# Optimization experiments

Hardware: AMD Instinct MI355X
Metric: run time of the kernel (lower is better)

Reference implementation:

```python
import jax, jax.numpy as jnp
import numpy as np

N, A, B, K = 100000, 64, 128, 27  # active sites, in/out channels, 3^3 offsets
EPS = 1e-4  # scn BatchNorm default eps
LEAK = 0.0  # leakiness=0 -> ReLU


def bn_lrelu(x, gamma, beta):
    # training-mode BN over active sites, fused leaky relu
    mu = x.mean(0)
    var = x.var(0)
    xh = (x - mu) * jax.lax.rsqrt(var + EPS) * gamma + beta
    return jnp.where(xh > 0, xh, LEAK * xh)


def subconv(f, nbr, mask, W):
    # submanifold conv via rulebook: f [N,Cin], nbr [N,K], mask [N,K], W [K,Cin,Cout]
    out = jnp.zeros((f.shape[0], W.shape[2]), f.dtype)
    for k in range(W.shape[0]):  # fixed small set of kernel offsets
        g = jnp.where(mask[:, k:k + 1], f[nbr[:, k]], jnp.zeros((), f.dtype))
        out = out + g @ W[k]
    return out


def setup_inputs() -> dict:
    key = jax.random.key(0)
    ks = jax.random.split(key, 8)
    feat = jax.random.normal(ks[0], (N, A), jnp.float32)
    nbr = jax.random.randint(ks[1], (N, K), 0, N, jnp.int32)
    mask = jax.random.randint(ks[2], (N, K), 0, 2, jnp.int32).astype(bool)
    # self-connection at center offset is always valid in submanifold conv
    center = K // 2
    nbr = nbr.at[:, center].set(jnp.arange(N, dtype=jnp.int32))
    mask = mask.at[:, center].set(True)
    s1 = 1.0 / np.sqrt(K * A)
    s2 = 1.0 / np.sqrt(K * B)
    W1 = jax.random.normal(ks[3], (K, A, B), jnp.float32) * s1
    W2 = jax.random.normal(ks[4], (K, B, B), jnp.float32) * s2
    Wnin = jax.random.normal(ks[5], (A, B), jnp.float32) / np.sqrt(A)
    gamma1 = jnp.ones((A,), jnp.float32)
    beta1 = jnp.zeros((A,), jnp.float32)
    gamma2 = jnp.ones((B,), jnp.float32)
    beta2 = jnp.zeros((B,), jnp.float32)
    return {"feat": feat, "gamma1": gamma1, "beta1": beta1, "W1": W1,
            "gamma2": gamma2, "beta2": beta2, "W2": W2, "Wnin": Wnin,
            "nbr": nbr, "mask": mask}


def reference(feat, gamma1, beta1, W1, gamma2, beta2, W2, Wnin, nbr, mask):
    y1 = feat @ Wnin  # NetworkInNetwork shortcut (a != b)
    h = bn_lrelu(feat, gamma1, beta1)
    h = subconv(h, nbr, mask, W1)
    h = bn_lrelu(h, gamma2, beta2)
    y2 = subconv(h, nbr, mask, W2)
    return y1 + y2  # add_feature_planes
```

## Files before the change

### kernel.cpp

```cpp
#include <hip/hip_runtime.h>
#include <stdint.h>

#define CA 64
#define CB 128
#define KOFF 27
#define BN_EPS 1e-4f

typedef short bf16x8 __attribute__((ext_vector_type(8)));
typedef float f32x4 __attribute__((ext_vector_type(4)));
typedef unsigned int u32x4 __attribute__((ext_vector_type(4)));
typedef unsigned short u16x4 __attribute__((ext_vector_type(4)));

__device__ __forceinline__ unsigned short f2bf(float f) {
  union { float f; uint32_t u; } c; c.f = f;
  uint32_t u = c.u;
  return (unsigned short)((u + 0x7FFFu + ((u >> 16) & 1u)) >> 16);
}

__global__ void detect_mask_k(const unsigned char* __restrict__ m, int* flag) {
  unsigned v = 0;
  for (int i = threadIdx.x; i < 4096; i += 256)
    if (i & 3) v |= m[i];
  if (v) atomicOr(flag, 1);
}

__global__ void pack_mask_k(const void* __restrict__ mp, const int* __restrict__ flag,
                            uint32_t* __restrict__ bits, int n) {
  int i = blockIdx.x * blockDim.x + threadIdx.x;
  if (i >= n) return;
  uint32_t b = 0;
  if (*flag) {
    const unsigned char* m = (const unsigned char*)mp + (size_t)i * KOFF;
    for (int k = 0; k < KOFF; k++) b |= (m[k] ? 1u : 0u) << k;
  } else {
    const int* m = (const int*)mp + (size_t)i * KOFF;
    for (int k = 0; k < KOFF; k++) b |= (m[k] ? 1u : 0u) << k;
  }
  bits[i] = b;
}

__global__ void transpose_w_k(const float* __restrict__ w, unsigned short* __restrict__ wt,
                              int K, int Cin, int Cout) {
  int idx = blockIdx.x * blockDim.x + threadIdx.x;
  int total = K * Cin * Cout;
  if (idx >= total) return;
  int ci = idx % Cin;
  int t2 = idx / Cin;
  int co = t2 % Cout;
  int k  = t2 / Cout;
  wt[idx] = f2bf(w[((size_t)k * Cin + ci) * Cout + co]);
}

template<int C>
__global__ void col_stats_k(const float* __restrict__ x, int n, float* __restrict__ sums) {
  __shared__ float ssum[C], ssq[C];
  int t = threadIdx.x;
  for (int i = t; i < C; i += 256) { ssum[i] = 0.f; ssq[i] = 0.f; }
  __syncthreads();
  const int c = t % C;
  const int rpb = 256 / C;
  float s = 0.f, q = 0.f;
  for (int r = blockIdx.x * rpb + t / C; r < n; r += gridDim.x * rpb) {
    float v = x[(size_t)r * C + c];
    s += v; q += v * v;
  }
  atomicAdd(&ssum[c], s);
  atomicAdd(&ssq[c], q);
  __syncthreads();
  for (int i = t; i < C; i += 256) {
    atomicAdd(&sums[i], ssum[i]);
    atomicAdd(&sums[C + i], ssq[i]);
  }
}

template<int C>
__global__ void bn_finalize_k(const float* __restrict__ sums, const float* __restrict__ gamma,
                              const float* __restrict__ beta, float* __restrict__ sc, int n) {
  int c = threadIdx.x;
  if (c >= C) return;
  float inv_n = 1.f / (float)n;
  float mean = sums[c] * inv_n;
  float var = sums[C + c] * inv_n - mean * mean;
  float rstd = rsqrtf(var + BN_EPS);
  float scale = gamma[c] * rstd;
  sc[c] = scale;
  sc[C + c] = beta[c] - mean * scale;
}

template<int C, bool RAW>
__global__ void bn_apply_k(const float* __restrict__ x, const float* __restrict__ sc,
                           unsigned short* __restrict__ h, unsigned short* __restrict__ raw,
                           int total) {
  int idx = (blockIdx.x * blockDim.x + threadIdx.x) * 4;
  if (idx >= total) return;
  f32x4 v = *(const f32x4*)&x[idx];
  int c0 = idx % C;
  u16x4 ho, ro;
#pragma unroll
  for (int j = 0; j < 4; j++) {
    float s = sc[c0 + j], b = sc[C + c0 + j];
    float hv = fmaxf(v[j] * s + b, 0.f);
    ho[j] = f2bf(hv);
    if (RAW) ro[j] = f2bf(v[j]);
  }
  *(u16x4*)&h[idx] = ho;
  if (RAW) *(u16x4*)&raw[idx] = ro;
}

template<int CIN, bool FUSE>
__launch_bounds__(256)
__global__ void conv_k(const unsigned short* __restrict__ hin,
                       const unsigned short* __restrict__ wt,
                       const int* __restrict__ nbr,
                       const uint32_t* __restrict__ mbits,
                       const unsigned short* __restrict__ fbraw,
                       const unsigned short* __restrict__ wnt,
                       float* __restrict__ out, int n) {
  constexpr int TR = 64;
  constexpr int STR = CIN + 8;
  constexpr int FSTR = CA + 8;
  __shared__ alignas(16) unsigned short tile[TR * STR];
  __shared__ alignas(16) unsigned short ftile[FUSE ? TR * FSTR : 16];
  __shared__ int lnbr[TR * KOFF];
  __shared__ uint32_t lmb[TR];

  const int t = threadIdx.x;
  const int rowbase = blockIdx.x * TR;
  const int nrows = min(TR, n - rowbase);

  for (int i = t; i < nrows * KOFF; i += 256) lnbr[i] = nbr[(size_t)rowbase * KOFF + i];
  if (t < TR) lmb[t] = (t < nrows) ? mbits[rowbase + t] : 0u;

  if constexpr (FUSE) {
#pragma unroll
    for (int p = 0; p < 2; p++) {
      int r = p * 32 + (t >> 3);
      int ch = (t & 7) * 8;
      u32x4 v = {0, 0, 0, 0};
      if (r < nrows) v = *(const u32x4*)&fbraw[(size_t)(rowbase + r) * CA + ch];
      *(u32x4*)&ftile[r * FSTR + ch] = v;
    }
  }
  __syncthreads();

  const int lane = t & 63;
  const int wave = t >> 6;
  const int l16 = lane & 15;
  const int quad = lane >> 4;
  const int colbase = wave * 32;

  f32x4 zero = {0.f, 0.f, 0.f, 0.f};
  f32x4 acc[4][2];
#pragma unroll
  for (int i = 0; i < 4; i++) { acc[i][0] = zero; acc[i][1] = zero; }

  if constexpr (FUSE) {
#pragma unroll
    for (int ks = 0; ks < CA / 32; ks++) {
      bf16x8 b0 = *(const bf16x8*)&wnt[(size_t)(colbase + l16) * CA + ks * 32 + quad * 8];
      bf16x8 b1 = *(const bf16x8*)&wnt[(size_t)(colbase + 16 + l16) * CA + ks * 32 + quad * 8];
#pragma unroll
      for (int rt = 0; rt < 4; rt++) {
        bf16x8 a = *(const bf16x8*)&ftile[(rt * 16 + l16) * FSTR + ks * 32 + quad * 8];
        acc[rt][0] = __builtin_amdgcn_mfma_f32_16x16x32_bf16(a, b0, acc[rt][0], 0, 0, 0);
        acc[rt][1] = __builtin_amdgcn_mfma_f32_16x16x32_bf16(a, b1, acc[rt][1], 0, 0, 0);
      }
    }
  }

  constexpr int CH = CIN / 8;
  constexpr int RPP = 256 / CH;

  for (int k = 0; k < KOFF; k++) {
#pragma unroll
    for (int p = 0; p < TR / RPP; p++) {
      int r = p * RPP + t / CH;
      int ch = (t % CH) * 8;
      u32x4 v = {0, 0, 0, 0};
      if (r < nrows && ((lmb[r] >> k) & 1u)) {
        int nb = lnbr[r * KOFF + k];
        v = *(const u32x4*)&hin[(size_t)nb * CIN + ch];
      }
      *(u32x4*)&tile[r * STR + ch] = v;
    }
    __syncthreads();
    const unsigned short* wk = wt + (size_t)k * CB * CIN;
#pragma unroll
    for (int ks = 0; ks < CIN / 32; ks++) {
      bf16x8 b0 = *(const bf16x8*)&wk[(size_t)(colbase + l16) * CIN + ks * 32 + quad * 8];
      bf16x8 b1 = *(const bf16x8*)&wk[(size_t)(colbase + 16 + l16) * CIN + ks * 32 + quad * 8];
#pragma unroll
      for (int rt = 0; rt < 4; rt++) {
        bf16x8 a = *(const bf16x8*)&tile[(rt * 16 + l16) * STR + ks * 32 + quad * 8];
        acc[rt][0] = __builtin_amdgcn_mfma_f32_16x16x32_bf16(a, b0, acc[rt][0], 0, 0, 0);
        acc[rt][1] = __builtin_amdgcn_mfma_f32_16x16x32_bf16(a, b1, acc[rt][1], 0, 0, 0);
      }
    }
    __syncthreads();
  }

#pragma unroll
  for (int rt = 0; rt < 4; rt++) {
#pragma unroll
    for (int ct = 0; ct < 2; ct++) {
#pragma unroll
      for (int i = 0; i < 4; i++) {
        int r = rt * 16 + quad * 4 + i;
        if (r < nrows) {
          int c = colbase + ct * 16 + l16;
          out[(size_t)(rowbase + r) * CB + c] = acc[rt][ct][i];
        }
      }
    }
  }
}

extern "C" void kernel_launch(void* const* d_in, const int* in_sizes, int n_in,
                              void* d_out, int out_size, void* d_ws, size_t ws_size,
                              hipStream_t stream) {
  const float* feat   = (const float*)d_in[0];
  const float* gamma1 = (const float*)d_in[1];
  const float* beta1  = (const float*)d_in[2];
  const float* W1     = (const float*)d_in[3];
  const float* gamma2 = (const float*)d_in[4];
  const float* beta2  = (const float*)d_in[5];
  const float* W2     = (const float*)d_in[6];
  const float* Wnin   = (const float*)d_in[7];
  const int*   nbr    = (const int*)d_in[8];
  const void*  mask   = d_in[9];
  float* out = (float*)d_out;

  const int n = in_sizes[0] / CA;

  char* ws = (char*)d_ws;
  size_t off = 0;
  auto alloc = [&](size_t bytes) { size_t p = off; off += (bytes + 255) & ~(size_t)255; return p; };
  int*            flag  = (int*)           (ws + alloc(256));
  float*          sums1 = (float*)         (ws + alloc(2 * CA * 4));
  float*          sums2 = (float*)         (ws + alloc(2 * CB * 4));
  float*          sc1   = (float*)         (ws + alloc(2 * CA * 4));
  float*          sc2   = (float*)         (ws + alloc(2 * CB * 4));
  uint32_t*       mbits = (uint32_t*)      (ws + alloc((size_t)n * 4));
  unsigned short* fb    = (unsigned short*)(ws + alloc((size_t)n * CA * 2));
  unsigned short* hb1   = (unsigned short*)(ws + alloc((size_t)n * CA * 2));
  float*          out1  = (float*)         (ws + alloc((size_t)n * CB * 4));
  unsigned short* hb2   = (unsigned short*)(ws + alloc((size_t)n * CB * 2));
  unsigned short* w1t   = (unsigned short*)(ws + alloc((size_t)KOFF * CB * CA * 2));
  unsigned short* w2t   = (unsigned short*)(ws + alloc((size_t)KOFF * CB * CB * 2));
  unsigned short* wnt   = (unsigned short*)(ws + alloc((size_t)CB * CA * 2));

  hipMemsetAsync(d_ws, 0, 1792, stream);

  detect_mask_k<<<1, 256, 0, stream>>>((const unsigned char*)mask, flag);
  pack_mask_k<<<(n + 255) / 256, 256, 0, stream>>>(mask, flag, mbits, n);

  {
    int t1 = KOFF * CA * CB, t2 = KOFF * CB * CB, t3 = CA * CB;
    transpose_w_k<<<(t1 + 255) / 256, 256, 0, stream>>>(W1, w1t, KOFF, CA, CB);
    transpose_w_k<<<(t2 + 255) / 256, 256, 0, stream>>>(W2, w2t, KOFF, CB, CB);
    transpose_w_k<<<(t3 + 255) / 256, 256, 0, stream>>>(Wnin, wnt, 1, CA, CB);
  }

  col_stats_k<CA><<<256, 256, 0, stream>>>(feat, n, sums1);
  bn_finalize_k<CA><<<1, CA, 0, stream>>>(sums1, gamma1, beta1, sc1, n);
  bn_apply_k<CA, true><<<(n * CA / 4 + 255) / 256, 256, 0, stream>>>(feat, sc1, hb1, fb, n * CA);

  conv_k<CA, false><<<(n + 63) / 64, 256, 0, stream>>>(hb1, w1t, nbr, mbits, nullptr, nullptr, out1, n);

  col_stats_k<CB><<<256, 256, 0, stream>>>(out1, n, sums2);
  bn_finalize_k<CB><<<1, CB, 0, stream>>>(sums2, gamma2, beta2, sc2, n);
  bn_apply_k<CB, false><<<(n * CB / 4 + 255) / 256, 256, 0, stream>>>(out1, sc2, hb2, nullptr, n * CB);

  conv_k<CB, true><<<(n + 63) / 64, 256, 0, stream>>>(hb2, w2t, nbr, mbits, fb, wnt, out, n);
}
```

Before: 606.5 us.

## Double-buffer gather tiles and prefetch weights in registers in sparse conv

The conv kernel now double-buffers the LDS gather tile. The neighbour rows for offset k+2 and the weight fragments for the next offsets are loaded into registers while the MFMAs for offset k run, so one barrier per offset replaces two. The barrier is a custom s_waitcnt lgkmcnt(0) plus s_barrier. This aims to hide the global gather and weight-load latency behind compute, at the cost of more registers and LDS that may lower occupancy. The three weight transpose launches are also merged into one kernel to cut launch overhead.

Result: faster. 531.1 us (-12.4%).

```diff
diff --git a/kernel.cpp b/kernel.cpp
--- a/kernel.cpp
+++ b/kernel.cpp
@@ -15,6 +15,10 @@
   union { float f; uint32_t u; } c; c.f = f;
   uint32_t u = c.u;
   return (unsigned short)((u + 0x7FFFu + ((u >> 16) & 1u)) >> 16);
+}
+
+__device__ __forceinline__ void barrier_lds() {
+  asm volatile("s_waitcnt lgkmcnt(0)\n\ts_barrier" ::: "memory");
 }
 
 __global__ void detect_mask_k(const unsigned char* __restrict__ m, int* flag) {
@@ -39,16 +43,24 @@
   bits[i] = b;
 }
 
-__global__ void transpose_w_k(const float* __restrict__ w, unsigned short* __restrict__ wt,
-                              int K, int Cin, int Cout) {
+__global__ void transpose_all_k(const float* __restrict__ W1, const float* __restrict__ W2,
+                                const float* __restrict__ Wnin,
+                                unsigned short* __restrict__ w1t, unsigned short* __restrict__ w2t,
+                                unsigned short* __restrict__ wnt) {
+  const int t1 = KOFF * CA * CB, t2 = KOFF * CB * CB, t3 = CA * CB;
   int idx = blockIdx.x * blockDim.x + threadIdx.x;
-  int total = K * Cin * Cout;
-  if (idx >= total) return;
-  int ci = idx % Cin;
-  int t2 = idx / Cin;
-  int co = t2 % Cout;
-  int k  = t2 / Cout;
-  wt[idx] = f2bf(w[((size_t)k * Cin + ci) * Cout + co]);
+  if (idx < t1) {
+    int ci = idx % CA; int r = idx / CA; int co = r % CB; int k = r / CB;
+    w1t[idx] = f2bf(W1[((size_t)k * CA + ci) * CB + co]);
+  } else if (idx < t1 + t2) {
+    int j = idx - t1;
+    int ci = j % CB; int r = j / CB; int co = r % CB; int k = r / CB;
+    w2t[j] = f2bf(W2[((size_t)k * CB + ci) * CB + co]);
+  } else if (idx < t1 + t2 + t3) {
+    int j = idx - t1 - t2;
+    int ci = j % CA; int co = j / CA;
+    wnt[j] = f2bf(Wnin[(size_t)ci * CB + co]);
+  }
 }
 
 template<int C>
@@ -119,7 +131,11 @@
   constexpr int TR = 64;
   constexpr int STR = CIN + 8;
   constexpr int FSTR = CA + 8;
-  __shared__ alignas(16) unsigned short tile[TR * STR];
+  constexpr int NKS = CIN / 32;
+  constexpr int CH = CIN / 8;
+  constexpr int NP = TR * CH / 256;
+
+  __shared__ alignas(16) unsigned short tile[2][TR * STR];
   __shared__ alignas(16) unsigned short ftile[FUSE ? TR * FSTR : 16];
   __shared__ int lnbr[TR * KOFF];
   __shared__ uint32_t lmb[TR];
@@ -148,17 +164,57 @@
   const int l16 = lane & 15;
   const int quad = lane >> 4;
   const int colbase = wave * 32;
-
-  f32x4 zero = {0.f, 0.f, 0.f, 0.f};
+  const int goff = (t % CH) * 8;
+  const int grow = t / CH;
+  const int boff0 = (colbase + l16) * CIN + quad * 8;
+  const int boff1 = boff0 + 16 * CIN;
+
   f32x4 acc[4][2];
 #pragma unroll
-  for (int i = 0; i < 4; i++) { acc[i][0] = zero; acc[i][1] = zero; }
+  for (int i = 0; i < 4; i++) { acc[i][0] = f32x4{0,0,0,0}; acc[i][1] = f32x4{0,0,0,0}; }
+
+  bf16x8 bfr[2][2 * NKS];
+  u32x4 gr[NP];
+
+#pragma unroll
+  for (int ks = 0; ks < NKS; ks++) {
+    bfr[0][2 * ks]     = *(const bf16x8*)&wt[boff0 + ks * 32];
+    bfr[0][2 * ks + 1] = *(const bf16x8*)&wt[boff1 + ks * 32];
+  }
+#pragma unroll
+  for (int p = 0; p < NP; p++) {
+    int r = p * (256 / CH) + grow;
+    u32x4 v = {0, 0, 0, 0};
+    if (r < nrows && (lmb[r] & 1u)) v = *(const u32x4*)&hin[(size_t)lnbr[r * KOFF] * CIN + goff];
+    gr[p] = v;
+  }
+#pragma unroll
+  for (int p = 0; p < NP; p++) {
+    int r = p * (256 / CH) + grow;
+    *(u32x4*)&tile[0][r * STR + goff] = gr[p];
+  }
+  {
+    const unsigned short* wk = wt + (size_t)1 * CB * CIN;
+#pragma unroll
+    for (int ks = 0; ks < NKS; ks++) {
+      bfr[1][2 * ks]     = *(const bf16x8*)&wk[boff0 + ks * 32];
+      bfr[1][2 * ks + 1] = *(const bf16x8*)&wk[boff1 + ks * 32];
+    }
+  }
+#pragma unroll
+  for (int p = 0; p < NP; p++) {
+    int r = p * (256 / CH) + grow;
+    u32x4 v = {0, 0, 0, 0};
+    if (r < nrows && ((lmb[r] >> 1) & 1u))
+      v = *(const u32x4*)&hin[(size_t)lnbr[r * KOFF + 1] * CIN + goff];
+    gr[p] = v;
+  }
 
   if constexpr (FUSE) {
 #pragma unroll
     for (int ks = 0; ks < CA / 32; ks++) {
-      bf16x8 b0 = *(const bf16x8*)&wnt[(size_t)(colbase + l16) * CA + ks * 32 + quad * 8];
-      bf16x8 b1 = *(const bf16x8*)&wnt[(size_t)(colbase + 16 + l16) * CA + ks * 32 + quad * 8];
+      bf16x8 b0 = *(const bf16x8*)&wnt[(colbase + l16) * CA + ks * 32 + quad * 8];
+      bf16x8 b1 = *(const bf16x8*)&wnt[(colbase + 16 + l16) * CA + ks * 32 + quad * 8];
 #pragma unroll
       for (int rt = 0; rt < 4; rt++) {
         bf16x8 a = *(const bf16x8*)&ftile[(rt * 16 + l16) * FSTR + ks * 32 + quad * 8];
@@ -167,36 +223,46 @@
       }
     }
   }
-
-  constexpr int CH = CIN / 8;
-  constexpr int RPP = 256 / CH;
-
+  barrier_lds();
+
+#pragma unroll
   for (int k = 0; k < KOFF; k++) {
-#pragma unroll
-    for (int p = 0; p < TR / RPP; p++) {
-      int r = p * RPP + t / CH;
-      int ch = (t % CH) * 8;
-      u32x4 v = {0, 0, 0, 0};
-      if (r < nrows && ((lmb[r] >> k) & 1u)) {
-        int nb = lnbr[r * KOFF + k];
-        v = *(const u32x4*)&hin[(size_t)nb * CIN + ch];
-      }
-      *(u32x4*)&tile[r * STR + ch] = v;
-    }
-    __syncthreads();
-    const unsigned short* wk = wt + (size_t)k * CB * CIN;
-#pragma unroll
-    for (int ks = 0; ks < CIN / 32; ks++) {
-      bf16x8 b0 = *(const bf16x8*)&wk[(size_t)(colbase + l16) * CIN + ks * 32 + quad * 8];
-      bf16x8 b1 = *(const bf16x8*)&wk[(size_t)(colbase + 16 + l16) * CIN + ks * 32 + quad * 8];
+    const int cur = k & 1, nxt = cur ^ 1;
+#pragma unroll
+    for (int ks = 0; ks < NKS; ks++) {
 #pragma unroll
       for (int rt = 0; rt < 4; rt++) {
-        bf16x8 a = *(const bf16x8*)&tile[(rt * 16 + l16) * STR + ks * 32 + quad * 8];
-        acc[rt][0] = __builtin_amdgcn_mfma_f32_16x16x32_bf16(a, b0, acc[rt][0], 0, 0, 0);
-        acc[rt][1] = __builtin_amdgcn_mfma_f32_16x16x32_bf16(a, b1, acc[rt][1], 0, 0, 0);
-      }
-    }
-    __syncthreads();
+        bf16x8 a = *(const bf16x8*)&tile[cur][(rt * 16 + l16) * STR + ks * 32 + quad * 8];
+        acc[rt][0] = __builtin_amdgcn_mfma_f32_16x16x32_bf16(a, bfr[cur][2 * ks],     acc[rt][0], 0, 0, 0);
+        acc[rt][1] = __builtin_amdgcn_mfma_f32_16x16x32_bf16(a, bfr[cur][2 * ks + 1], acc[rt][1], 0, 0, 0);
+      }
+    }
+    if (k + 2 < KOFF) {
+      const unsigned short* wk = wt + (size_t)(k + 2) * CB * CIN;
+#pragma unroll
+      for (int ks = 0; ks < NKS; ks++) {
+        bfr[cur][2 * ks]     = *(const bf16x8*)&wk[boff0 + ks * 32];
+        bfr[cur][2 * ks + 1] = *(const bf16x8*)&wk[boff1 + ks * 32];
+      }
+    }
+    if (k + 1 < KOFF) {
+#pragma unroll
+      for (int p = 0; p < NP; p++) {
+        int r = p * (256 / CH) + grow;
+        *(u32x4*)&tile[nxt][r * STR + goff] = gr[p];
+      }
+      if (k + 2 < KOFF) {
+#pragma unroll
+        for (int p = 0; p < NP; p++) {
+          int r = p * (256 / CH) + grow;
+          u32x4 v = {0, 0, 0, 0};
+          if (r < nrows && ((lmb[r] >> (k + 2)) & 1u))
+            v = *(const u32x4*)&hin[(size_t)lnbr[r * KOFF + k + 2] * CIN + goff];
+          gr[p] = v;
+        }
+      }
+      barrier_lds();
+    }
   }
 
 #pragma unroll
@@ -255,10 +321,8 @@
   pack_mask_k<<<(n + 255) / 256, 256, 0, stream>>>(mask, flag, mbits, n);
 
   {
-    int t1 = KOFF * CA * CB, t2 = KOFF * CB * CB, t3 = CA * CB;
-    transpose_w_k<<<(t1 + 255) / 256, 256, 0, stream>>>(W1, w1t, KOFF, CA, CB);
-    transpose_w_k<<<(t2 + 255) / 256, 256, 0, stream>>>(W2, w2t, KOFF, CB, CB);
-    transpose_w_k<<<(t3 + 255) / 256, 256, 0, stream>>>(Wnin, wnt, 1, CA, CB);
+    int tot = KOFF * CA * CB + KOFF * CB * CB + CA * CB;
+    transpose_all_k<<<(tot + 255) / 256, 256, 0, stream>>>(W1, W2, Wnin, w1t, w2t, wnt);
   }
 
   col_stats_k<CA><<<256, 256, 0, stream>>>(feat, n, sums1);
```
